# Kernel tuning notes

Hardware: AMD Instinct MI355X
Metric: run time of the kernel (lower is better)

Reference implementation:

```python
import jax, jax.numpy as jnp
import numpy as np

THRESHOLD = 0.2  # relation_threshold default
LN_EPS = 1e-5


def setup_inputs() -> dict:
    key = jax.random.key(0)
    ks = jax.random.split(key, 4)
    N1, N2, F, H, R = 256, 256, 512, 512, 4
    feats_img = jax.random.normal(ks[0], (N1, F), dtype=jnp.float32)
    feats_txt = jax.random.normal(ks[1], (N2, F), dtype=jnp.float32)
    # relation_projector params (R stacked copies of the 2-layer MLP)
    W1 = jax.random.normal(ks[2], (R, H, 2 * F), dtype=jnp.float32) / np.sqrt(2 * F)
    b1 = jnp.zeros((R, H), dtype=jnp.float32)
    gamma = jnp.ones((R, H), dtype=jnp.float32)
    beta = jnp.zeros((R, H), dtype=jnp.float32)
    w2 = jax.random.normal(ks[3], (R, H), dtype=jnp.float32) / np.sqrt(H)
    b2 = jnp.zeros((R,), dtype=jnp.float32)
    return {"feats_img": feats_img, "feats_txt": feats_txt, "W1": W1, "b1": b1,
            "gamma": gamma, "beta": beta, "w2": w2, "b2": b2}


def _relation_scores(x, W1, b1, gamma, beta, w2, b2):
    """Vectorized pairwise MLP: for each relation r, score[i,j] = MLP_r(cat(x_i, x_j)).
    Returns [N, N, R]."""
    N, F = x.shape
    R = W1.shape[0]
    Wl, Wr = W1[:, :, :F], W1[:, :, F:]  # Linear on concat = left half @ x_i + right half @ x_j
    scores = []
    for r in range(R):  # small fixed loop over relations keeps peak memory at one [N,N,H] block
        a = x @ Wl[r].T                                  # [N, H]
        b = x @ Wr[r].T                                  # [N, H]
        h = a[:, None, :] + b[None, :, :] + b1[r]        # [N, N, H]
        mu = h.mean(-1, keepdims=True)
        var = h.var(-1, keepdims=True)                   # biased var, matches torch LayerNorm
        hn = (h - mu) * jax.lax.rsqrt(var + LN_EPS) * gamma[r] + beta[r]
        s = jnp.maximum(hn, 0.0) @ w2[r] + b2[r]         # [N, N]
        scores.append(s)
    return jnp.stack(scores, axis=-1)                    # [N, N, R]


def reference(feats_img, feats_txt, W1, b1, gamma, beta, w2, b2):
    # node_features = cat over modalities (node_types is a static host-side list: omitted)
    x = jnp.concatenate([feats_img, feats_txt], axis=0)  # [N, F]
    S = _relation_scores(x, W1, b1, gamma, beta, w2, b2) # [N, N, R]
    best_rel = jnp.argmax(S, axis=-1).astype(jnp.int32)  # edge_types, dense form
    best_score = S.max(axis=-1)                          # edge_weights, dense form
    N = x.shape[0]
    diag = jnp.eye(N, dtype=bool)
    edge_mask = (~diag) & (best_score > THRESHOLD)       # dense encoding of edge_index
    return x, best_score, best_rel, edge_mask
```

## Files before the change

### kernel.cpp

```cpp
#include <hip/hip_runtime.h>
#include <math.h>


namespace {
constexpr size_t PLANE  = 512 * 512;
constexpr size_t OFF_A   = 0;
constexpr size_t OFF_B   = OFF_A + 4 * PLANE;
constexpr size_t OFF_DOT = OFF_B + 4 * PLANE;
constexpr size_t OFF_S   = OFF_DOT + 8 * PLANE;
constexpr size_t OFF_MA  = OFF_S + 8 * PLANE;
constexpr size_t OFF_QA  = OFF_MA + 2048;
constexpr size_t OFF_MB  = OFF_QA + 2048;
constexpr size_t OFF_QB  = OFF_MB + 2048;
constexpr size_t OFF_G   = OFF_QB + 2048;
constexpr size_t OFF_BW  = OFF_G + 2048;
}

__global__ __launch_bounds__(256) void k0_gemm(const float* __restrict__ img,
                                               const float* __restrict__ txt,
                                               const float* __restrict__ W1,
                                               const float* __restrict__ b1,
                                               float* __restrict__ ws) {
  const int b = blockIdx.x;
  const int it = b >> 6;
  const int ct = b & 63;
  const int which = ct >> 5;
  const int r = (ct >> 3) & 3;
  const int ht = ct & 7;
  const int i0 = it << 6, h0 = ht << 6;
  const int t = threadIdx.x;
  const int tx = t & 15, ty = t >> 4;

  __shared__ float Xs[16 * 68];
  __shared__ float Wsm[16 * 68];

  float acc[16], pacc[16];
#pragma unroll
  for (int p = 0; p < 16; ++p) { acc[p] = 0.f; pacc[p] = 0.f; }

  const int srow = t >> 2;
  const int sf4 = (t & 3) << 2;
  const int xi = i0 + srow;
  const float* xrow = (xi < 256) ? (img + (size_t)xi * 512)
                                 : (txt + (size_t)(xi - 256) * 512);
  const float* wrow = W1 + (size_t)(r * 512 + h0 + srow) * 1024 + which * 512;

  for (int k0 = 0; k0 < 512; k0 += 16) {
    const float4 xv = *(const float4*)(xrow + k0 + sf4);
    const float4 wv = *(const float4*)(wrow + k0 + sf4);
    __syncthreads();
    Xs[(sf4 + 0) * 68 + srow] = xv.x;
    Xs[(sf4 + 1) * 68 + srow] = xv.y;
    Xs[(sf4 + 2) * 68 + srow] = xv.z;
    Xs[(sf4 + 3) * 68 + srow] = xv.w;
    Wsm[(sf4 + 0) * 68 + srow] = wv.x;
    Wsm[(sf4 + 1) * 68 + srow] = wv.y;
    Wsm[(sf4 + 2) * 68 + srow] = wv.z;
    Wsm[(sf4 + 3) * 68 + srow] = wv.w;
    __syncthreads();
#pragma unroll
    for (int k = 0; k < 16; ++k) {
      const float4 a4 = *(const float4*)&Xs[k * 68 + 4 * ty];
      const float4 b4 = *(const float4*)&Wsm[k * 68 + 4 * tx];
      const float av[4] = {a4.x, a4.y, a4.z, a4.w};
      const float bv[4] = {b4.x, b4.y, b4.z, b4.w};
#pragma unroll
      for (int c = 0; c < 4; ++c)
#pragma unroll
        for (int d = 0; d < 4; ++d)
          pacc[c * 4 + d] = fmaf(av[c], bv[d], pacc[c * 4 + d]);
    }
#pragma unroll
    for (int p = 0; p < 16; ++p) { acc[p] += pacc[p]; pacc[p] = 0.f; }
  }

  float4 bb = make_float4(0.f, 0.f, 0.f, 0.f);
  if (which) bb = *(const float4*)(b1 + r * 512 + h0 + 4 * tx);
  float* dst = ws + (which ? OFF_B : OFF_A) + (size_t)r * PLANE;
#pragma unroll
  for (int c = 0; c < 4; ++c) {
    float4 v;
    v.x = acc[c * 4 + 0] + bb.x;
    v.y = acc[c * 4 + 1] + bb.y;
    v.z = acc[c * 4 + 2] + bb.z;
    v.w = acc[c * 4 + 3] + bb.w;
    *(float4*)(dst + (size_t)(i0 + 4 * ty + c) * 512 + h0 + 4 * tx) = v;
  }
}

__global__ __launch_bounds__(256) void k1_stats(float* __restrict__ ws,
                                                const float* __restrict__ gamma,
                                                const float* __restrict__ beta,
                                                const float* __restrict__ w2) {
  const int t = threadIdx.x;
  const int gw = (blockIdx.x * 256 + t) >> 6;
  const int lane = t & 63;
  const int which = gw >> 11;
  const int rr = (gw >> 9) & 3;
  const int row = gw & 511;
  const float* src =
      ws + (which ? OFF_B : OFF_A) + (size_t)(rr * 512 + row) * 512 + lane * 8;
  float s = 0.f, q = 0.f;
#pragma unroll
  for (int c = 0; c < 2; ++c) {
    const float4 v = *(const float4*)(src + c * 4);
    s += v.x + v.y + v.z + v.w;
    q += v.x * v.x + v.y * v.y + v.z * v.z + v.w * v.w;
  }
#pragma unroll
  for (int off = 32; off >= 1; off >>= 1) {
    s += __shfl_down(s, off, 64);
    q += __shfl_down(q, off, 64);
  }
  if (lane == 0) {
    ws[(which ? OFF_MB : OFF_MA) + rr * 512 + row] = s * (1.f / 512.f);
    ws[(which ? OFF_QB : OFF_QA) + rr * 512 + row] = q;
  }
  if (blockIdx.x < 8) {
    const int idx = blockIdx.x * 256 + t;
    ws[OFF_G + idx] = gamma[idx];
    float2 bw;
    bw.x = beta[idx];
    bw.y = w2[idx];
    *(float2*)(ws + OFF_BW + (size_t)idx * 2) = bw;
  }
}

__global__ __launch_bounds__(256) void k2_dot(float* __restrict__ ws) {
  const int b = blockIdx.x;
  const int jt = b & 7, it = (b >> 3) & 7, r = (b >> 6) & 3, ks = b >> 8;
  const int i0 = it << 6, j0 = jt << 6;
  const int kb = ks << 8;
  const int t = threadIdx.x;
  const int tx = t & 15, ty = t >> 4;

  __shared__ float As[16 * 68];
  __shared__ float Bs[16 * 68];

  float acc[16];
#pragma unroll
  for (int p = 0; p < 16; ++p) acc[p] = 0.f;

  const int srow = t >> 2, sf4 = (t & 3) << 2;
  const float* arow = ws + OFF_A + (size_t)(r * 512 + i0 + srow) * 512 + kb;
  const float* brow = ws + OFF_B + (size_t)(r * 512 + j0 + srow) * 512 + kb;

  for (int k0 = 0; k0 < 256; k0 += 16) {
    const float4 av = *(const float4*)(arow + k0 + sf4);
    const float4 bv = *(const float4*)(brow + k0 + sf4);
    __syncthreads();
    As[(sf4 + 0) * 68 + srow] = av.x;
    As[(sf4 + 1) * 68 + srow] = av.y;
    As[(sf4 + 2) * 68 + srow] = av.z;
    As[(sf4 + 3) * 68 + srow] = av.w;
    Bs[(sf4 + 0) * 68 + srow] = bv.x;
    Bs[(sf4 + 1) * 68 + srow] = bv.y;
    Bs[(sf4 + 2) * 68 + srow] = bv.z;
    Bs[(sf4 + 3) * 68 + srow] = bv.w;
    __syncthreads();
#pragma unroll
    for (int k = 0; k < 16; ++k) {
      const float4 a4 = *(const float4*)&As[k * 68 + 4 * ty];
      const float4 b4 = *(const float4*)&Bs[k * 68 + 4 * tx];
      const float av2[4] = {a4.x, a4.y, a4.z, a4.w};
      const float bv2[4] = {b4.x, b4.y, b4.z, b4.w};
#pragma unroll
      for (int c = 0; c < 4; ++c)
#pragma unroll
        for (int d = 0; d < 4; ++d)
          acc[c * 4 + d] = fmaf(av2[c], bv2[d], acc[c * 4 + d]);
    }
  }
  float* dst = ws + OFF_DOT + (size_t)ks * (4 * PLANE) + (size_t)r * PLANE;
#pragma unroll
  for (int c = 0; c < 4; ++c) {
    float4 v;
    v.x = acc[c * 4 + 0]; v.y = acc[c * 4 + 1];
    v.z = acc[c * 4 + 2]; v.w = acc[c * 4 + 3];
    *(float4*)(dst + (size_t)(i0 + 4 * ty + c) * 512 + j0 + 4 * tx) = v;
  }
}

__global__ __launch_bounds__(512) void k3_score(float* __restrict__ ws) {
  const int b = blockIdx.x;
  const int jt = b & 7, it = (b >> 3) & 7, r = (b >> 6) & 3, ks = b >> 8;
  const int i0 = it << 6, j0 = jt << 6;
  const int t = threadIdx.x;
  const int tx = t & 31, ty = t >> 5;

  __shared__ float As2[64 * 68];
  __shared__ float Bs2[64 * 68];
  __shared__ float bwS[64 * 2];

  const float4 mav = *(const float4*)(ws + OFF_MA + r * 512 + i0 + 4 * ty);
  const float4 qav = *(const float4*)(ws + OFF_QA + r * 512 + i0 + 4 * ty);
  const float2 mbv = *(const float2*)(ws + OFF_MB + r * 512 + j0 + 2 * tx);
  const float2 qbv = *(const float2*)(ws + OFF_QB + r * 512 + j0 + 2 * tx);
  const float mavA[4] = {mav.x, mav.y, mav.z, mav.w};
  const float qavA[4] = {qav.x, qav.y, qav.z, qav.w};
  const float mbA[2] = {mbv.x, mbv.y};
  const float qbA[2] = {qbv.x, qbv.y};
  float Sv[8], acc[8];
#pragma unroll
  for (int c = 0; c < 4; ++c) {
    const size_t doff = (size_t)r * PLANE + (size_t)(i0 + 4 * ty + c) * 512 + j0 + 2 * tx;
    const float2 d0 = *(const float2*)(ws + OFF_DOT + doff);
    const float2 d1 = *(const float2*)(ws + OFF_DOT + 4 * PLANE + doff);
    const float dA[2] = {d0.x + d1.x, d0.y + d1.y};
#pragma unroll
    for (int d = 0; d < 2; ++d) {
      const int p = c * 2 + d;
      const float mu = mavA[c] + mbA[d];
      const float msq = (qavA[c] + qbA[d] + 2.f * dA[d]) * (1.f / 512.f);
      const float var = msq - mu * mu;
      Sv[p] = 1.0f / sqrtf(var + 1e-5f);
      acc[p] = 0.f;
    }
  }

  const int kbase = ks << 8;
  const int srow = t >> 4, sf4 = (t & 15) << 2;
  const int ra = i0 + srow, rb = j0 + srow;
  const float maA2[2] = {ws[OFF_MA + r * 512 + ra], ws[OFF_MA + r * 512 + ra + 32]};
  const float mbA2[2] = {ws[OFF_MB + r * 512 + rb], ws[OFF_MB + r * 512 + rb + 32]};

  for (int kc = 0; kc < 4; ++kc) {
    const int kb = kbase + (kc << 6);
    const float4 gv = *(const float4*)(ws + OFF_G + r * 512 + kb + sf4);
    float4 avs[2], bvs[2];
#pragma unroll
    for (int c2 = 0; c2 < 2; ++c2) {
      avs[c2] = *(const float4*)(ws + OFF_A + (size_t)(r * 512 + ra + 32 * c2) * 512 + kb + sf4);
      bvs[c2] = *(const float4*)(ws + OFF_B + (size_t)(r * 512 + rb + 32 * c2) * 512 + kb + sf4);
    }
    float2 bwv = make_float2(0.f, 0.f);
    if (t < 64) bwv = *(const float2*)(ws + OFF_BW + (size_t)(r * 512 + kb + t) * 2);
    __syncthreads();
    {
      const float ga[4] = {gv.x, gv.y, gv.z, gv.w};
#pragma unroll
      for (int c2 = 0; c2 < 2; ++c2) {
        const int row = srow + 32 * c2;
        const float aq[4] = {avs[c2].x, avs[c2].y, avs[c2].z, avs[c2].w};
        const float bq[4] = {bvs[c2].x, bvs[c2].y, bvs[c2].z, bvs[c2].w};
#pragma unroll
        for (int q = 0; q < 4; ++q) {
          As2[(sf4 + q) * 68 + row] = (aq[q] - maA2[c2]) * ga[q];
          Bs2[(sf4 + q) * 68 + row] = (bq[q] - mbA2[c2]) * ga[q];
        }
      }
    }
    if (t < 64) *(float2*)(bwS + 2 * t) = bwv;
    __syncthreads();

    float cacc[8];
#pragma unroll
    for (int p = 0; p < 8; ++p) cacc[p] = 0.f;

#pragma unroll 8
    for (int k = 0; k < 64; ++k) {
      const float4 aA = *(const float4*)&As2[k * 68 + 4 * ty];
      const float2 bB = *(const float2*)&Bs2[k * 68 + 2 * tx];
      const float2 bw = *(const float2*)&bwS[2 * k];
      const float aq[4] = {aA.x, aA.y, aA.z, aA.w};
      const float bq[2] = {bB.x, bB.y};
#pragma unroll
      for (int c = 0; c < 4; ++c)
#pragma unroll
        for (int d = 0; d < 2; ++d) {
          const int p = c * 2 + d;
          const float u = aq[c] + bq[d];
          const float hn = fmaf(u, Sv[p], bw.x);
          const float m = fmaxf(hn, 0.f);
          cacc[p] = fmaf(m, bw.y, cacc[p]);
        }
    }
#pragma unroll
    for (int p = 0; p < 8; ++p) acc[p] += cacc[p];
  }

  float* dst = ws + OFF_S + (size_t)ks * (4 * PLANE) + (size_t)r * PLANE;
#pragma unroll
  for (int c = 0; c < 4; ++c) {
    float2 v;
    v.x = acc[c * 2 + 0];
    v.y = acc[c * 2 + 1];
    *(float2*)(dst + (size_t)(i0 + 4 * ty + c) * 512 + j0 + 2 * tx) = v;
  }
}

__global__ __launch_bounds__(256) void k4_combine(const float* __restrict__ ws,
                                                  const float* __restrict__ img,
                                                  const float* __restrict__ txt,
                                                  const float* __restrict__ b2,
                                                  float* __restrict__ out) {
  const int idx = blockIdx.x * 256 + threadIdx.x;
  const int i = idx >> 9, j = idx & 511;
  const float* s0 = ws + OFF_S;
  const float* s1 = ws + OFF_S + 4 * PLANE;
  float best = -3.4e38f;
  int rel = 0;
#pragma unroll
  for (int r = 0; r < 4; ++r) {
    const float s = s0[r * PLANE + idx] + s1[r * PLANE + idx] + b2[r];
    if (s > best) { best = s; rel = r; }
  }
  out[idx] = (i < 256) ? img[idx] : txt[idx - 131072];
  out[PLANE + idx] = best;
  out[2 * PLANE + idx] = (float)rel;
  out[3 * PLANE + idx] = (i != j && (double)best > 0.2) ? 1.0f : 0.0f;
}

extern "C" void kernel_launch(void* const* d_in, const int* in_sizes, int n_in,
                              void* d_out, int out_size, void* d_ws, size_t ws_size,
                              hipStream_t stream) {
  const float* img   = (const float*)d_in[0];
  const float* txt   = (const float*)d_in[1];
  const float* W1    = (const float*)d_in[2];
  const float* b1    = (const float*)d_in[3];
  const float* gamma = (const float*)d_in[4];
  const float* beta  = (const float*)d_in[5];
  const float* w2    = (const float*)d_in[6];
  const float* b2    = (const float*)d_in[7];
  float* ws  = (float*)d_ws;
  float* out = (float*)d_out;
  (void)in_sizes; (void)n_in; (void)out_size; (void)ws_size;

  hipLaunchKernelGGL(k0_gemm,    dim3(512),  dim3(256), 0, stream, img, txt, W1, b1, ws);
  hipLaunchKernelGGL(k1_stats,   dim3(1024), dim3(256), 0, stream, ws, gamma, beta, w2);
  hipLaunchKernelGGL(k2_dot,     dim3(512),  dim3(256), 0, stream, ws);
  hipLaunchKernelGGL(k3_score,   dim3(512),  dim3(512), 0, stream, ws);
  hipLaunchKernelGGL(k4_combine, dim3(1024), dim3(256), 0, stream, ws, img, txt, b2, out);
}
```

Baseline: 198.9 us.

## Enlarge k3_score per-thread tile, prefetch next K chunk, swizzle shared memory

```diff
diff --git a/kernel.cpp b/kernel.cpp
--- a/kernel.cpp
+++ b/kernel.cpp
@@ -181,12 +181,12 @@
   }
 }
 
-__global__ __launch_bounds__(512) void k3_score(float* __restrict__ ws) {
+__global__ __launch_bounds__(256) void k3_score(float* __restrict__ ws) {
   const int b = blockIdx.x;
   const int jt = b & 7, it = (b >> 3) & 7, r = (b >> 6) & 3, ks = b >> 8;
   const int i0 = it << 6, j0 = jt << 6;
   const int t = threadIdx.x;
-  const int tx = t & 31, ty = t >> 5;
+  const int tx = t & 15, ty = t >> 4;
 
   __shared__ float As2[64 * 68];
   __shared__ float Bs2[64 * 68];
@@ -194,22 +194,22 @@
 
   const float4 mav = *(const float4*)(ws + OFF_MA + r * 512 + i0 + 4 * ty);
   const float4 qav = *(const float4*)(ws + OFF_QA + r * 512 + i0 + 4 * ty);
-  const float2 mbv = *(const float2*)(ws + OFF_MB + r * 512 + j0 + 2 * tx);
-  const float2 qbv = *(const float2*)(ws + OFF_QB + r * 512 + j0 + 2 * tx);
+  const float4 mbv = *(const float4*)(ws + OFF_MB + r * 512 + j0 + 4 * tx);
+  const float4 qbv = *(const float4*)(ws + OFF_QB + r * 512 + j0 + 4 * tx);
   const float mavA[4] = {mav.x, mav.y, mav.z, mav.w};
   const float qavA[4] = {qav.x, qav.y, qav.z, qav.w};
-  const float mbA[2] = {mbv.x, mbv.y};
-  const float qbA[2] = {qbv.x, qbv.y};
-  float Sv[8], acc[8];
+  const float mbA[4] = {mbv.x, mbv.y, mbv.z, mbv.w};
+  const float qbA[4] = {qbv.x, qbv.y, qbv.z, qbv.w};
+  float Sv[16], acc[16];
 #pragma unroll
   for (int c = 0; c < 4; ++c) {
-    const size_t doff = (size_t)r * PLANE + (size_t)(i0 + 4 * ty + c) * 512 + j0 + 2 * tx;
-    const float2 d0 = *(const float2*)(ws + OFF_DOT + doff);
-    const float2 d1 = *(const float2*)(ws + OFF_DOT + 4 * PLANE + doff);
-    const float dA[2] = {d0.x + d1.x, d0.y + d1.y};
-#pragma unroll
-    for (int d = 0; d < 2; ++d) {
-      const int p = c * 2 + d;
+    const size_t doff = (size_t)r * PLANE + (size_t)(i0 + 4 * ty + c) * 512 + j0 + 4 * tx;
+    const float4 d0 = *(const float4*)(ws + OFF_DOT + doff);
+    const float4 d1 = *(const float4*)(ws + OFF_DOT + 4 * PLANE + doff);
+    const float dA[4] = {d0.x + d1.x, d0.y + d1.y, d0.z + d1.z, d0.w + d1.w};
+#pragma unroll
+    for (int d = 0; d < 4; ++d) {
+      const int p = c * 4 + d;
       const float mu = mavA[c] + mbA[d];
       const float msq = (qavA[c] + qbA[d] + 2.f * dA[d]) * (1.f / 512.f);
       const float var = msq - mu * mu;
@@ -219,56 +219,77 @@
   }
 
   const int kbase = ks << 8;
-  const int srow = t >> 4, sf4 = (t & 15) << 2;
-  const int ra = i0 + srow, rb = j0 + srow;
-  const float maA2[2] = {ws[OFF_MA + r * 512 + ra], ws[OFF_MA + r * 512 + ra + 32]};
-  const float mbA2[2] = {ws[OFF_MB + r * 512 + rb], ws[OFF_MB + r * 512 + rb + 32]};
-
+  const int srow = ty;
+  const int sf4 = tx << 2;
+  const int sblk = tx & 7;
+  float maR[4], mbR[4];
+#pragma unroll
+  for (int c2 = 0; c2 < 4; ++c2) {
+    maR[c2] = ws[OFF_MA + r * 512 + i0 + srow + 16 * c2];
+    mbR[c2] = ws[OFF_MB + r * 512 + j0 + srow + 16 * c2];
+  }
+
+  float4 aC[4], bC[4], gC;
+  float2 bwC = make_float2(0.f, 0.f);
+  {
+    const int kb = kbase;
+    gC = *(const float4*)(ws + OFF_G + r * 512 + kb + sf4);
+#pragma unroll
+    for (int c2 = 0; c2 < 4; ++c2) {
+      aC[c2] = *(const float4*)(ws + OFF_A + (size_t)(r * 512 + i0 + srow + 16 * c2) * 512 + kb + sf4);
+      bC[c2] = *(const float4*)(ws + OFF_B + (size_t)(r * 512 + j0 + srow + 16 * c2) * 512 + kb + sf4);
+    }
+    if (t < 64) bwC = *(const float2*)(ws + OFF_BW + (size_t)(r * 512 + kb + t) * 2);
+  }
+
+#pragma unroll
   for (int kc = 0; kc < 4; ++kc) {
-    const int kb = kbase + (kc << 6);
-    const float4 gv = *(const float4*)(ws + OFF_G + r * 512 + kb + sf4);
-    float4 avs[2], bvs[2];
-#pragma unroll
-    for (int c2 = 0; c2 < 2; ++c2) {
-      avs[c2] = *(const float4*)(ws + OFF_A + (size_t)(r * 512 + ra + 32 * c2) * 512 + kb + sf4);
-      bvs[c2] = *(const float4*)(ws + OFF_B + (size_t)(r * 512 + rb + 32 * c2) * 512 + kb + sf4);
-    }
-    float2 bwv = make_float2(0.f, 0.f);
-    if (t < 64) bwv = *(const float2*)(ws + OFF_BW + (size_t)(r * 512 + kb + t) * 2);
     __syncthreads();
     {
-      const float ga[4] = {gv.x, gv.y, gv.z, gv.w};
-#pragma unroll
-      for (int c2 = 0; c2 < 2; ++c2) {
-        const int row = srow + 32 * c2;
-        const float aq[4] = {avs[c2].x, avs[c2].y, avs[c2].z, avs[c2].w};
-        const float bq[4] = {bvs[c2].x, bvs[c2].y, bvs[c2].z, bvs[c2].w};
+      const float ga[4] = {gC.x, gC.y, gC.z, gC.w};
+#pragma unroll
+      for (int c2 = 0; c2 < 4; ++c2) {
+        const int row = srow + 16 * c2;
+        const int off = (((row >> 2) ^ sblk) << 2) + (row & 3);
+        const float aq[4] = {aC[c2].x, aC[c2].y, aC[c2].z, aC[c2].w};
+        const float bq[4] = {bC[c2].x, bC[c2].y, bC[c2].z, bC[c2].w};
 #pragma unroll
         for (int q = 0; q < 4; ++q) {
-          As2[(sf4 + q) * 68 + row] = (aq[q] - maA2[c2]) * ga[q];
-          Bs2[(sf4 + q) * 68 + row] = (bq[q] - mbA2[c2]) * ga[q];
+          As2[(sf4 + q) * 68 + off] = (aq[q] - maR[c2]) * ga[q];
+          Bs2[(sf4 + q) * 68 + off] = (bq[q] - mbR[c2]) * ga[q];
         }
       }
-    }
-    if (t < 64) *(float2*)(bwS + 2 * t) = bwv;
-    __syncthreads();
-
-    float cacc[8];
-#pragma unroll
-    for (int p = 0; p < 8; ++p) cacc[p] = 0.f;
-
-#pragma unroll 8
+      if (t < 64) *(float2*)(bwS + 2 * t) = bwC;
+    }
+    if (kc < 3) {
+      const int kb = kbase + ((kc + 1) << 6);
+      gC = *(const float4*)(ws + OFF_G + r * 512 + kb + sf4);
+#pragma unroll
+      for (int c2 = 0; c2 < 4; ++c2) {
+        aC[c2] = *(const float4*)(ws + OFF_A + (size_t)(r * 512 + i0 + srow + 16 * c2) * 512 + kb + sf4);
+        bC[c2] = *(const float4*)(ws + OFF_B + (size_t)(r * 512 + j0 + srow + 16 * c2) * 512 + kb + sf4);
+      }
+      if (t < 64) bwC = *(const float2*)(ws + OFF_BW + (size_t)(r * 512 + kb + t) * 2);
+    }
+    __syncthreads();
+
+    float cacc[16];
+#pragma unroll
+    for (int p = 0; p < 16; ++p) cacc[p] = 0.f;
+
+#pragma unroll 4
     for (int k = 0; k < 64; ++k) {
-      const float4 aA = *(const float4*)&As2[k * 68 + 4 * ty];
-      const float2 bB = *(const float2*)&Bs2[k * 68 + 2 * tx];
+      const int K = (k >> 2) & 7;
+      const float4 aA = *(const float4*)&As2[k * 68 + ((ty ^ K) << 2)];
+      const float4 bB = *(const float4*)&Bs2[k * 68 + ((tx ^ K) << 2)];
       const float2 bw = *(const float2*)&bwS[2 * k];
       const float aq[4] = {aA.x, aA.y, aA.z, aA.w};
-      const float bq[2] = {bB.x, bB.y};
+      const float bq[4] = {bB.x, bB.y, bB.z, bB.w};
 #pragma unroll
       for (int c = 0; c < 4; ++c)
 #pragma unroll
-        for (int d = 0; d < 2; ++d) {
-          const int p = c * 2 + d;
+        for (int d = 0; d < 4; ++d) {
+          const int p = c * 4 + d;
           const float u = aq[c] + bq[d];
           const float hn = fmaf(u, Sv[p], bw.x);
           const float m = fmaxf(hn, 0.f);
@@ -276,16 +297,18 @@
         }
     }
 #pragma unroll
-    for (int p = 0; p < 8; ++p) acc[p] += cacc[p];
+    for (int p = 0; p < 16; ++p) acc[p] += cacc[p];
   }
 
   float* dst = ws + OFF_S + (size_t)ks * (4 * PLANE) + (size_t)r * PLANE;
 #pragma unroll
   for (int c = 0; c < 4; ++c) {
-    float2 v;
-    v.x = acc[c * 2 + 0];
-    v.y = acc[c * 2 + 1];
-    *(float2*)(dst + (size_t)(i0 + 4 * ty + c) * 512 + j0 + 2 * tx) = v;
+    float4 v;
+    v.x = acc[c * 4 + 0];
+    v.y = acc[c * 4 + 1];
+    v.z = acc[c * 4 + 2];
+    v.w = acc[c * 4 + 3];
+    *(float4*)(dst + (size_t)(i0 + 4 * ty + c) * 512 + j0 + 4 * tx) = v;
   }
 }
 
@@ -329,6 +352,6 @@
   hipLaunchKernelGGL(k0_gemm,    dim3(512),  dim3(256), 0, stream, img, txt, W1, b1, ws);
   hipLaunchKernelGGL(k1_stats,   dim3(1024), dim3(256), 0, stream, ws, gamma, beta, w2);
   hipLaunchKernelGGL(k2_dot,     dim3(512),  dim3(256), 0, stream, ws);
-  hipLaunchKernelGGL(k3_score,   dim3(512),  dim3(512), 0, stream, ws);
+  hipLaunchKernelGGL(k3_score,   dim3(512),  dim3(256), 0, stream, ws);
   hipLaunchKernelGGL(k4_combine, dim3(1024), dim3(256), 0, stream, ws, img, txt, b2, out);
 }
```

After: 194.6 us. 1.02x faster.
